# Kernel tuning notes

Hardware: AMD Instinct MI355X
Metric: run time of the kernel (lower is better)

The kernel has to match this reference:

```python
import jax, jax.numpy as jnp
import numpy as np

B = 16384       # batch
G = 8           # groups
S = 16          # state_c (per-group in/out channels)
H = 512         # hidden_c (per-group hidden channels)
FACTOR = 1.0
SWISH_DIV = 1.1


def setup_inputs() -> dict:
    key = jax.random.key(0)
    ks = jax.random.split(key, 12)
    def w(k, shape, fan_in):
        bound = 1.0 / np.sqrt(fan_in)
        return jax.random.uniform(k, shape, jnp.float32, -bound, bound)
    return {
        "x":  jax.random.normal(ks[0], (B, G * S), dtype=jnp.float32),
        # grouped 1x1 convs as per-group linear weights [G, out_c, in_c]
        "W1": w(ks[1], (G, H, S), S), "b1": w(ks[2], (G, H), S),
        "beta1": jnp.full((G,), 0.5, jnp.float32),
        "W2": w(ks[3], (G, H, H), H), "b2": w(ks[4], (G, H), H),
        "beta2": jnp.full((G,), 0.5, jnp.float32),
        "W3": w(ks[5], (G, H, H), H), "b3": w(ks[6], (G, H), H),
        "beta3": jnp.full((G,), 0.5, jnp.float32),
        "W4": w(ks[7], (G, S, H), H), "b4": w(ks[8], (G, S), H),
    }


def _group_swish(x, beta):
    # x: [B, G, C]; beta: [G] -> y = x * sigmoid(x * softplus(beta)) / 1.1
    sp = jax.nn.softplus(beta)[None, :, None]
    return x * jax.nn.sigmoid(x * sp) / SWISH_DIV


def reference(x, W1, b1, beta1, W2, b2, beta2, W3, b3, beta3, W4, b4):
    h = x.reshape(-1, G, S)                                   # [B,G,S]
    h = jnp.einsum('bgs,ghs->bgh', h, W1) + b1[None]          # [B,G,H]
    h = _group_swish(h, beta1)
    h = jnp.einsum('bgi,goi->bgo', h, W2) + b2[None]
    h = _group_swish(h, beta2)
    h = jnp.einsum('bgi,goi->bgo', h, W3) + b3[None]
    h = _group_swish(h, beta3)
    h = jnp.einsum('bgh,gsh->bgs', h, W4) + b4[None]          # [B,G,S]
    return h.reshape(-1, G * S) * FACTOR
```

## Files before the change

kernel.cpp:

```cpp
#include <hip/hip_runtime.h>
#include <stdint.h>

#define G_ 8
#define S_ 16
#define H_ 512
#define TB 128
#define NTH 512

typedef _Float16 h16;
typedef _Float16 h16x8 __attribute__((ext_vector_type(8)));
typedef float f32x4 __attribute__((ext_vector_type(4)));
typedef float f32x16 __attribute__((ext_vector_type(16)));

#define HB_BYTES (TB * 1024)
#define XB_BYTES (TB * 32)
#define SMEM_BYTES (HB_BYTES + XB_BYTES)


__device__ __forceinline__ float swishf(float v, float sp) {
    const float e = __expf(-v * sp);
    return v * __builtin_amdgcn_rcpf(1.0f + e) * (1.0f / 1.1f);
}

__device__ __forceinline__ uint32_t pk16(float a, float b) {
    return __builtin_bit_cast(uint32_t, __builtin_amdgcn_cvt_pkrtz(a, b));
}

template<bool USEWS>
__device__ __forceinline__ h16x8 loadA32ks(const h16* __restrict__ wpk,
                                           const float* __restrict__ wf,
                                           int ks, int nb, int ln, int Ksrc) {
    if constexpr (USEWS) {
        return *(const h16x8*)(wpk + (((size_t)ks * 16 + nb) * 64 + ln) * 8);
    } else {
        const int row = nb * 32 + (ln & 31);
        const int k = ks * 16 + (ln >> 5) * 8;
        const float* p = wf + (size_t)row * Ksrc + k;
        h16x8 r;
        #pragma unroll
        for (int j = 0; j < 8; ++j) r[j] = (h16)p[j];
        return r;
    }
}

template<bool USEWS>
__device__ __forceinline__ h16x8 loadA16(const h16* __restrict__ wpk,
                                         const float* __restrict__ wf,
                                         int ks32, int ln, int Ksrc) {
    if constexpr (USEWS) {
        return *(const h16x8*)(wpk + ((size_t)ks32 * 64 + ln) * 8);
    } else {
        const int row = ln & 15;
        const int k = ks32 * 32 + (ln >> 4) * 8;
        const float* p = wf + (size_t)row * Ksrc + k;
        h16x8 r;
        #pragma unroll
        for (int j = 0; j < 8; ++j) r[j] = (h16)p[j];
        return r;
    }
}

__device__ __forceinline__ void swish_store32(const f32x16 (&acc)[2][4], char* hb,
                                              const float* __restrict__ bias, float sp,
                                              int wv, int ln) {
    const int l31 = ln & 31, lh = ln >> 5;
    char* const wbase = hb + wv * 16384 + l31 * 16 + lh * 8;
    #pragma unroll
    for (int ot = 0; ot < 2; ++ot) {
        #pragma unroll
        for (int rq = 0; rq < 4; ++rq) {
            const int col0 = wv * 64 + ot * 32 + rq * 8 + lh * 4;
            const f32x4 bv = *(const f32x4*)(bias + col0);
            #pragma unroll
            for (int bt = 0; bt < 4; ++bt) {
                const float v0 = swishf(acc[ot][bt][rq * 4 + 0] + bv[0], sp);
                const float v1 = swishf(acc[ot][bt][rq * 4 + 1] + bv[1], sp);
                const float v2 = swishf(acc[ot][bt][rq * 4 + 2] + bv[2], sp);
                const float v3 = swishf(acc[ot][bt][rq * 4 + 3] + bv[3], sp);
                const uint64_t u = (uint64_t)pk16(v0, v1)
                                 | ((uint64_t)pk16(v2, v3) << 32);
                *(uint64_t*)(wbase + (ot * 4 + rq) * 2048 + bt * 512) = u;
            }
        }
    }
}

template<bool USEWS>
__device__ __forceinline__ void layerH32(f32x16 (&acc)[2][4],
                                         const h16* __restrict__ wpk, const float* __restrict__ wf,
                                         const char* __restrict__ hb, int wv, int ln) {
    const int l31 = ln & 31, lh = ln >> 5;
    const char* const bbase = hb + l31 * 16 + lh * 2048;
    const int nb0 = wv * 2;
    #pragma unroll
    for (int ot = 0; ot < 2; ++ot)
        #pragma unroll
        for (int bt = 0; bt < 4; ++bt) acc[ot][bt] = (f32x16)(0.f);

    #pragma unroll 2
    for (int ks = 0; ks < 32; ++ks) {
        const h16x8 a0 = loadA32ks<USEWS>(wpk, wf, ks, nb0 + 0, ln, H_);
        const h16x8 a1 = loadA32ks<USEWS>(wpk, wf, ks, nb0 + 1, ln, H_);
        h16x8 b[4];
        #pragma unroll
        for (int bt = 0; bt < 4; ++bt)
            b[bt] = *(const h16x8*)(bbase + ks * 4096 + bt * 512);
        __builtin_amdgcn_s_setprio(1);
        #pragma unroll
        for (int bt = 0; bt < 4; ++bt) {
            acc[0][bt] = __builtin_amdgcn_mfma_f32_32x32x16_f16(a0, b[bt], acc[0][bt], 0, 0, 0);
            acc[1][bt] = __builtin_amdgcn_mfma_f32_32x32x16_f16(a1, b[bt], acc[1][bt], 0, 0, 0);
        }
        __builtin_amdgcn_s_setprio(0);
    }
}

template<bool USEWS>
__global__ __launch_bounds__(NTH, 2) void mlp_fused(
    const float* __restrict__ x,
    const float* __restrict__ W1f, const float* __restrict__ b1, const float* __restrict__ be1,
    const float* __restrict__ W2f, const float* __restrict__ b2, const float* __restrict__ be2,
    const float* __restrict__ W3f, const float* __restrict__ b3, const float* __restrict__ be3,
    const float* __restrict__ W4f, const float* __restrict__ b4,
    const h16* __restrict__ W1p, const h16* __restrict__ W2p,
    const h16* __restrict__ W3p, const h16* __restrict__ W4p,
    float* __restrict__ out) {
    extern __shared__ char smem[];
    char* __restrict__ xb = smem + HB_BYTES;

    const int bid = blockIdx.x;
    const int g = bid & 7;
    const int rowbase = (bid >> 3) * TB;
    const int tid = threadIdx.x;
    const int wv = tid >> 6;
    const int ln = tid & 63;
    const int l31 = ln & 31;
    const int lh = ln >> 5;

    const float sp1 = log1pf(__expf(be1[g]));
    const float sp2 = log1pf(__expf(be2[g]));
    const float sp3 = log1pf(__expf(be3[g]));

    const h16* w1p = W1p + (size_t)g * H_ * S_;
    const h16* w2p = W2p + (size_t)g * H_ * H_;
    const h16* w3p = W3p + (size_t)g * H_ * H_;
    const h16* w4p = W4p + (size_t)g * S_ * H_;
    const float* w1f = W1f + (size_t)g * H_ * S_;
    const float* w2f = W2f + (size_t)g * H_ * H_;
    const float* w3f = W3f + (size_t)g * H_ * H_;
    const float* w4f = W4f + (size_t)g * S_ * H_;

    {
        const int idx = tid * 4;
        const int r = idx >> 4, s = idx & 15;
        const f32x4 v = *(const f32x4*)(x + (size_t)(rowbase + r) * (G_ * S_) + g * S_ + s);
        const uint64_t u = (uint64_t)pk16(v[0], v[1]) | ((uint64_t)pk16(v[2], v[3]) << 32);
        *(uint64_t*)(xb + (s >> 3) * 2048 + r * 16 + (s & 7) * 2) = u;
    }
    __syncthreads();

    f32x16 acc[2][4];

    {
        #pragma unroll
        for (int ot = 0; ot < 2; ++ot)
            #pragma unroll
            for (int bt = 0; bt < 4; ++bt) acc[ot][bt] = (f32x16)(0.f);
        const char* const xbase = xb + l31 * 16 + lh * 2048;
        const h16x8 aW0 = loadA32ks<USEWS>(w1p, w1f, 0, wv * 2 + 0, ln, S_);
        const h16x8 aW1 = loadA32ks<USEWS>(w1p, w1f, 0, wv * 2 + 1, ln, S_);
        #pragma unroll
        for (int bt = 0; bt < 4; ++bt) {
            const h16x8 bX = *(const h16x8*)(xbase + bt * 512);
            acc[0][bt] = __builtin_amdgcn_mfma_f32_32x32x16_f16(aW0, bX, acc[0][bt], 0, 0, 0);
            acc[1][bt] = __builtin_amdgcn_mfma_f32_32x32x16_f16(aW1, bX, acc[1][bt], 0, 0, 0);
        }
    }
    swish_store32(acc, smem, b1 + g * H_, sp1, wv, ln);
    __syncthreads();

    layerH32<USEWS>(acc, w2p, w2f, smem, wv, ln);
    __syncthreads();
    swish_store32(acc, smem, b2 + g * H_, sp2, wv, ln);
    __syncthreads();

    layerH32<USEWS>(acc, w3p, w3f, smem, wv, ln);
    __syncthreads();
    swish_store32(acc, smem, b3 + g * H_, sp3, wv, ln);
    __syncthreads();

    {
        f32x4 a4 = {0.f, 0.f, 0.f, 0.f};
        const int l15 = ln & 15, lq = ln >> 4;
        const char* const b4base = smem + lq * 2048 + (wv * 16 + l15) * 16;
        #pragma unroll 4
        for (int ks = 0; ks < 16; ++ks) {
            const h16x8 a = loadA16<USEWS>(w4p, w4f, ks, ln, H_);
            const h16x8 b = *(const h16x8*)(b4base + ks * 8192);
            a4 = __builtin_amdgcn_mfma_f32_16x16x32_f16(a, b, a4, 0, 0, 0);
        }
        const int brow = wv * 16 + l15;
        const int s0 = lq * 4;
        const f32x4 bv = *(const f32x4*)(b4 + g * S_ + s0);
        f32x4 o4;
        #pragma unroll
        for (int r = 0; r < 4; ++r) o4[r] = a4[r] + bv[r];
        *(f32x4*)(out + (size_t)(rowbase + brow) * (G_ * S_) + g * S_ + s0) = o4;
    }
}

__global__ void packW32(const float* __restrict__ s, h16* __restrict__ d,
                        int KB, int Ks) {
    const int t = blockIdx.x * 256 + threadIdx.x;
    const int total = G_ * KB * 16 * 64;
    if (t >= total) return;
    const int ln = t & 63;
    const int blk = t >> 6;
    const int nb = blk & 15;
    const int rest = blk >> 4;
    const int ks = rest % KB;
    const int g = rest / KB;
    const int row = g * H_ + nb * 32 + (ln & 31);
    const int k = ks * 16 + (ln >> 5) * 8;
    const float* p = s + (size_t)row * Ks + k;
    h16x8 o;
    #pragma unroll
    for (int j = 0; j < 8; ++j) o[j] = (h16)p[j];
    *(h16x8*)(d + (size_t)t * 8) = o;
}

__global__ void packW16(const float* __restrict__ s, h16* __restrict__ d,
                        int NB_total, int KB, int Ks) {
    const int t = blockIdx.x * 256 + threadIdx.x;
    const int total = NB_total * KB * 64;
    if (t >= total) return;
    const int ln = t & 63;
    const int blk = t >> 6;
    const int kb = blk % KB;
    const int nbg = blk / KB;
    const int row = nbg * 16 + (ln & 15);
    const int k = kb * 32 + (ln >> 4) * 8;
    const float* p = s + (size_t)row * Ks + k;
    h16x8 o;
    #pragma unroll
    for (int j = 0; j < 8; ++j) o[j] = (h16)p[j];
    *(h16x8*)(d + (size_t)t * 8) = o;
}

extern "C" void kernel_launch(void* const* d_in, const int* in_sizes, int n_in,
                              void* d_out, int out_size, void* d_ws, size_t ws_size,
                              hipStream_t stream) {
    const float* x   = (const float*)d_in[0];
    const float* W1  = (const float*)d_in[1];
    const float* b1  = (const float*)d_in[2];
    const float* be1 = (const float*)d_in[3];
    const float* W2  = (const float*)d_in[4];
    const float* b2  = (const float*)d_in[5];
    const float* be2 = (const float*)d_in[6];
    const float* W3  = (const float*)d_in[7];
    const float* b3  = (const float*)d_in[8];
    const float* be3 = (const float*)d_in[9];
    const float* W4  = (const float*)d_in[10];
    const float* b4  = (const float*)d_in[11];
    float* out = (float*)d_out;

    const size_t nW2  = (size_t)G_ * H_ * H_;
    const size_t nW1p = (size_t)G_ * H_ * S_;
    const size_t nW4  = (size_t)G_ * S_ * H_;
    const size_t need = (2 * nW2 + nW1p + nW4) * sizeof(h16);

    const dim3 grid((16384 / TB) * G_), blk(NTH);

    if (ws_size >= need) {
        h16* W2p = (h16*)d_ws;
        h16* W3p = W2p + nW2;
        h16* W1p = W3p + nW2;
        h16* W4p = W1p + nW1p;
        packW32<<<dim3((unsigned)((nW2 / 8 + 255) / 256)), dim3(256), 0, stream>>>(W2, W2p, 32, H_);
        packW32<<<dim3((unsigned)((nW2 / 8 + 255) / 256)), dim3(256), 0, stream>>>(W3, W3p, 32, H_);
        packW32<<<dim3((unsigned)((nW1p / 8 + 255) / 256)), dim3(256), 0, stream>>>(W1, W1p, 1, S_);
        packW16<<<dim3((unsigned)((nW4 / 8 + 255) / 256)), dim3(256), 0, stream>>>(W4, W4p, G_, 16, H_);
        (void)hipFuncSetAttribute(reinterpret_cast<const void*>(mlp_fused<true>),
                                  hipFuncAttributeMaxDynamicSharedMemorySize, (int)SMEM_BYTES);
        mlp_fused<true><<<grid, blk, SMEM_BYTES, stream>>>(
            x, W1, b1, be1, W2, b2, be2, W3, b3, be3, W4, b4,
            W1p, W2p, W3p, W4p, out);
    } else {
        (void)hipFuncSetAttribute(reinterpret_cast<const void*>(mlp_fused<false>),
                                  hipFuncAttributeMaxDynamicSharedMemorySize, (int)SMEM_BYTES);
        mlp_fused<false><<<grid, blk, SMEM_BYTES, stream>>>(
            x, W1, b1, be1, W2, b2, be2, W3, b3, be3, W4, b4,
            nullptr, nullptr, nullptr, nullptr, out);
    }
}
```

Baseline: 206.5 us.

## Halve batch tile to 64 rows with 4 waves each computing 128 outputs

```diff
diff --git a/kernel.cpp b/kernel.cpp
--- a/kernel.cpp
+++ b/kernel.cpp
@@ -4,8 +4,8 @@
 #define G_ 8
 #define S_ 16
 #define H_ 512
-#define TB 128
-#define NTH 512
+#define TB 64
+#define NTH 256
 
 typedef _Float16 h16;
 typedef _Float16 h16x8 __attribute__((ext_vector_type(8)));
@@ -13,7 +13,7 @@
 typedef float f32x16 __attribute__((ext_vector_type(16)));
 
 #define HB_BYTES (TB * 1024)
-#define XB_BYTES (TB * 32)
+#define XB_BYTES 2048
 #define SMEM_BYTES (HB_BYTES + XB_BYTES)
 
 
@@ -60,56 +60,56 @@
     }
 }
 
-__device__ __forceinline__ void swish_store32(const f32x16 (&acc)[2][4], char* hb,
+__device__ __forceinline__ void swish_store32(const f32x16 (&acc)[4][2], char* hb,
                                               const float* __restrict__ bias, float sp,
                                               int wv, int ln) {
     const int l31 = ln & 31, lh = ln >> 5;
     char* const wbase = hb + wv * 16384 + l31 * 16 + lh * 8;
     #pragma unroll
-    for (int ot = 0; ot < 2; ++ot) {
+    for (int ot = 0; ot < 4; ++ot) {
         #pragma unroll
         for (int rq = 0; rq < 4; ++rq) {
-            const int col0 = wv * 64 + ot * 32 + rq * 8 + lh * 4;
+            const int col0 = wv * 128 + ot * 32 + rq * 8 + lh * 4;
             const f32x4 bv = *(const f32x4*)(bias + col0);
             #pragma unroll
-            for (int bt = 0; bt < 4; ++bt) {
+            for (int bt = 0; bt < 2; ++bt) {
                 const float v0 = swishf(acc[ot][bt][rq * 4 + 0] + bv[0], sp);
                 const float v1 = swishf(acc[ot][bt][rq * 4 + 1] + bv[1], sp);
                 const float v2 = swishf(acc[ot][bt][rq * 4 + 2] + bv[2], sp);
                 const float v3 = swishf(acc[ot][bt][rq * 4 + 3] + bv[3], sp);
                 const uint64_t u = (uint64_t)pk16(v0, v1)
                                  | ((uint64_t)pk16(v2, v3) << 32);
-                *(uint64_t*)(wbase + (ot * 4 + rq) * 2048 + bt * 512) = u;
+                *(uint64_t*)(wbase + (ot * 4 + rq) * 1024 + bt * 512) = u;
             }
         }
     }
 }
 
 template<bool USEWS>
-__device__ __forceinline__ void layerH32(f32x16 (&acc)[2][4],
+__device__ __forceinline__ void layerH32(f32x16 (&acc)[4][2],
                                          const h16* __restrict__ wpk, const float* __restrict__ wf,
                                          const char* __restrict__ hb, int wv, int ln) {
     const int l31 = ln & 31, lh = ln >> 5;
-    const char* const bbase = hb + l31 * 16 + lh * 2048;
-    const int nb0 = wv * 2;
-    #pragma unroll
-    for (int ot = 0; ot < 2; ++ot)
-        #pragma unroll
-        for (int bt = 0; bt < 4; ++bt) acc[ot][bt] = (f32x16)(0.f);
+    const char* const bbase = hb + l31 * 16 + lh * 1024;
+    const int nb0 = wv * 4;
+    #pragma unroll
+    for (int ot = 0; ot < 4; ++ot)
+        #pragma unroll
+        for (int bt = 0; bt < 2; ++bt) acc[ot][bt] = (f32x16)(0.f);
 
     #pragma unroll 2
     for (int ks = 0; ks < 32; ++ks) {
-        const h16x8 a0 = loadA32ks<USEWS>(wpk, wf, ks, nb0 + 0, ln, H_);
-        const h16x8 a1 = loadA32ks<USEWS>(wpk, wf, ks, nb0 + 1, ln, H_);
-        h16x8 b[4];
-        #pragma unroll
-        for (int bt = 0; bt < 4; ++bt)
-            b[bt] = *(const h16x8*)(bbase + ks * 4096 + bt * 512);
+        h16x8 a[4];
+        #pragma unroll
+        for (int ot = 0; ot < 4; ++ot)
+            a[ot] = loadA32ks<USEWS>(wpk, wf, ks, nb0 + ot, ln, H_);
+        const h16x8 b0 = *(const h16x8*)(bbase + ks * 2048);
+        const h16x8 b1 = *(const h16x8*)(bbase + ks * 2048 + 512);
         __builtin_amdgcn_s_setprio(1);
         #pragma unroll
-        for (int bt = 0; bt < 4; ++bt) {
-            acc[0][bt] = __builtin_amdgcn_mfma_f32_32x32x16_f16(a0, b[bt], acc[0][bt], 0, 0, 0);
-            acc[1][bt] = __builtin_amdgcn_mfma_f32_32x32x16_f16(a1, b[bt], acc[1][bt], 0, 0, 0);
+        for (int ot = 0; ot < 4; ++ot) {
+            acc[ot][0] = __builtin_amdgcn_mfma_f32_32x32x16_f16(a[ot], b0, acc[ot][0], 0, 0, 0);
+            acc[ot][1] = __builtin_amdgcn_mfma_f32_32x32x16_f16(a[ot], b1, acc[ot][1], 0, 0, 0);
         }
         __builtin_amdgcn_s_setprio(0);
     }
@@ -155,25 +155,25 @@
         const int r = idx >> 4, s = idx & 15;
         const f32x4 v = *(const f32x4*)(x + (size_t)(rowbase + r) * (G_ * S_) + g * S_ + s);
         const uint64_t u = (uint64_t)pk16(v[0], v[1]) | ((uint64_t)pk16(v[2], v[3]) << 32);
-        *(uint64_t*)(xb + (s >> 3) * 2048 + r * 16 + (s & 7) * 2) = u;
-    }
-    __syncthreads();
-
-    f32x16 acc[2][4];
+        *(uint64_t*)(xb + (s >> 3) * 1024 + r * 16 + (s & 7) * 2) = u;
+    }
+    __syncthreads();
+
+    f32x16 acc[4][2];
 
     {
         #pragma unroll
-        for (int ot = 0; ot < 2; ++ot)
+        for (int ot = 0; ot < 4; ++ot)
             #pragma unroll
-            for (int bt = 0; bt < 4; ++bt) acc[ot][bt] = (f32x16)(0.f);
-        const char* const xbase = xb + l31 * 16 + lh * 2048;
-        const h16x8 aW0 = loadA32ks<USEWS>(w1p, w1f, 0, wv * 2 + 0, ln, S_);
-        const h16x8 aW1 = loadA32ks<USEWS>(w1p, w1f, 0, wv * 2 + 1, ln, S_);
-        #pragma unroll
-        for (int bt = 0; bt < 4; ++bt) {
-            const h16x8 bX = *(const h16x8*)(xbase + bt * 512);
-            acc[0][bt] = __builtin_amdgcn_mfma_f32_32x32x16_f16(aW0, bX, acc[0][bt], 0, 0, 0);
-            acc[1][bt] = __builtin_amdgcn_mfma_f32_32x32x16_f16(aW1, bX, acc[1][bt], 0, 0, 0);
+            for (int bt = 0; bt < 2; ++bt) acc[ot][bt] = (f32x16)(0.f);
+        const char* const xbase = xb + l31 * 16 + lh * 1024;
+        const h16x8 bX0 = *(const h16x8*)(xbase);
+        const h16x8 bX1 = *(const h16x8*)(xbase + 512);
+        #pragma unroll
+        for (int ot = 0; ot < 4; ++ot) {
+            const h16x8 aW = loadA32ks<USEWS>(w1p, w1f, 0, wv * 4 + ot, ln, S_);
+            acc[ot][0] = __builtin_amdgcn_mfma_f32_32x32x16_f16(aW, bX0, acc[ot][0], 0, 0, 0);
+            acc[ot][1] = __builtin_amdgcn_mfma_f32_32x32x16_f16(aW, bX1, acc[ot][1], 0, 0, 0);
         }
     }
     swish_store32(acc, smem, b1 + g * H_, sp1, wv, ln);
@@ -192,11 +192,11 @@
     {
         f32x4 a4 = {0.f, 0.f, 0.f, 0.f};
         const int l15 = ln & 15, lq = ln >> 4;
-        const char* const b4base = smem + lq * 2048 + (wv * 16 + l15) * 16;
+        const char* const b4base = smem + lq * 1024 + (wv * 16 + l15) * 16;
         #pragma unroll 4
         for (int ks = 0; ks < 16; ++ks) {
             const h16x8 a = loadA16<USEWS>(w4p, w4f, ks, ln, H_);
-            const h16x8 b = *(const h16x8*)(b4base + ks * 8192);
+            const h16x8 b = *(const h16x8*)(b4base + ks * 4096);
             a4 = __builtin_amdgcn_mfma_f32_16x16x32_f16(a, b, a4, 0, 0, 0);
         }
         const int brow = wv * 16 + l15;
```

Measured after the change: 191.1 us. 7.5% less time.
